# Kernel tuning notes

Hardware: AMD Instinct MI355X
Metric: run time of the kernel (lower is better)

Reference implementation:

```python
import jax, jax.numpy as jnp
import numpy as np

N = 600_000            # active input voxels
CIN, COUT = 64, 128    # IN_CHANNELS, NUM_BEV_FEATURES
B, Z, Y, X = 4, 16, 468, 468  # sparse grid (Waymo-like); conv halves Z
BN_EPS = 1e-5


def setup_inputs() -> dict:
    rng = np.random.default_rng(0)
    # unique active voxel coordinates
    lin = rng.choice(B * Z * Y * X, size=N, replace=False)
    b = lin // (Z * Y * X)
    r = lin % (Z * Y * X)
    z = r // (Y * X)
    r = r % (Y * X)
    y = r // X
    x = r % X
    # spconv rulebook for kernel (2,1,1), stride (2,1,1), pad 0:
    # tap id along z and output segment id from unique (b, z//2, y, x)
    kz = (z % 2).astype(np.int32)
    keys = ((b * (Z // 2) + z // 2) * Y + y) * X + x
    _, inv = np.unique(keys, return_inverse=True)
    out_ids = inv.astype(np.int32)
    n_out = np.int32(out_ids.max() + 1)

    key = jax.random.key(0)
    ks = jax.random.split(key, 6)
    return {
        "features": jax.random.normal(ks[0], (N, CIN), dtype=jnp.float32),
        "W": jax.random.normal(ks[1], (2, CIN, COUT), dtype=jnp.float32) * 0.05,
        "gamma": jax.random.uniform(ks[2], (COUT,), dtype=jnp.float32, minval=0.5, maxval=1.5),
        "beta": jax.random.normal(ks[3], (COUT,), dtype=jnp.float32) * 0.1,
        "running_mean": jax.random.normal(ks[4], (COUT,), dtype=jnp.float32) * 0.1,
        "running_var": jax.random.uniform(ks[5], (COUT,), dtype=jnp.float32, minval=0.5, maxval=1.5),
        "kz": jnp.asarray(kz),
        "out_ids": jnp.asarray(out_ids),
        "n_out": jnp.asarray(n_out),
    }


def reference(features, W, gamma, beta, running_mean, running_var, kz, out_ids, n_out):
    # gather-GEMM: one GEMM per kernel tap, select by tap id
    y0 = features @ W[0]                       # [N, COUT]
    y1 = features @ W[1]
    contrib = jnp.where((kz == 0)[:, None], y0, y1)
    # scatter-add into output voxels (padded to N segments for static shape)
    out = jax.ops.segment_sum(contrib, out_ids, num_segments=N)  # [N, COUT]
    # BatchNorm1d (eval) + ReLU, fused into scatter output pass
    inv_std = gamma * jax.lax.rsqrt(running_var + BN_EPS)
    out = jax.nn.relu((out - running_mean) * inv_std + beta)
    # zero out padding rows beyond the true number of output voxels
    valid = (jnp.arange(N) < n_out)[:, None]
    return jnp.where(valid, out, 0.0)
```

## Files before the change

kernel.cpp:

```cpp
#include <hip/hip_runtime.h>
#include <stdint.h>

#define CIN 64
#define COUT 128
#define TILE_ROWS 64
#define BLOCK 256
#define WT_STRIDE 136
#define A_STRIDE 136

typedef __attribute__((ext_vector_type(8))) __bf16 bf16x8;
typedef __attribute__((ext_vector_type(8))) unsigned short ushort8;
typedef __attribute__((ext_vector_type(4))) float f32x4;

__device__ __forceinline__ unsigned short f2bf(float f) {
    uint32_t u = __float_as_uint(f);
    u = (u + 0x7FFFu + ((u >> 16) & 1u)) >> 16;
    return (unsigned short)u;
}

__global__ void scatter_inv_kernel(const int* __restrict__ kz,
                                   const int* __restrict__ oid,
                                   int* __restrict__ inv0,
                                   int* __restrict__ inv1,
                                   int n) {
    int i = blockIdx.x * blockDim.x + threadIdx.x;
    if (i < n) {
        int o = oid[i];
        if (kz[i] == 0) inv0[o] = i + 1;
        else            inv1[o] = i + 1;
    }
}

__launch_bounds__(BLOCK)
__global__ void spconv_bn_relu_kernel(const float* __restrict__ feat,
                                      const float* __restrict__ W,
                                      const float* __restrict__ gamma,
                                      const float* __restrict__ beta,
                                      const float* __restrict__ rmean,
                                      const float* __restrict__ rvar,
                                      const int* __restrict__ inv0,
                                      const int* __restrict__ inv1,
                                      const int* __restrict__ n_out_p,
                                      float* __restrict__ out,
                                      int N, int num_tiles) {
    __shared__ unsigned short lds_wT[COUT * WT_STRIDE];
    __shared__ unsigned short lds_a[TILE_ROWS * A_STRIDE];
    __shared__ float lds_scale[COUT];
    __shared__ float lds_bias[COUT];

    const int tid = threadIdx.x;
    const int nout = *n_out_p;

    const float4* W4 = (const float4*)W;
    #pragma unroll
    for (int u = 0; u < 16; ++u) {
        int flat4 = u * BLOCK + tid;
        int n4 = flat4 & 31;
        int k  = flat4 >> 5;
        float4 v = W4[flat4];
        int nb = n4 * 4;
        lds_wT[(nb + 0) * WT_STRIDE + k] = f2bf(v.x);
        lds_wT[(nb + 1) * WT_STRIDE + k] = f2bf(v.y);
        lds_wT[(nb + 2) * WT_STRIDE + k] = f2bf(v.z);
        lds_wT[(nb + 3) * WT_STRIDE + k] = f2bf(v.w);
    }
    if (tid < COUT) {
        float s = gamma[tid] * rsqrtf(rvar[tid] + 1e-5f);
        lds_scale[tid] = s;
        lds_bias[tid]  = fmaf(-rmean[tid], s, beta[tid]);
    }
    __syncthreads();

    const float4* feat4 = (const float4*)feat;
    const int wave = tid >> 6;
    const int lane = tid & 63;
    const int lrow = lane & 15;
    const int quad = lane >> 4;

    for (int tile = blockIdx.x; tile < num_tiles; tile += gridDim.x) {
        const int tile_base = tile * TILE_ROWS;

        #pragma unroll
        for (int u = 0; u < 8; ++u) {
            int flat  = u * BLOCK + tid;
            int r     = flat >> 5;
            int rem   = flat & 31;
            int tap   = rem >> 4;
            int chunk = rem & 15;
            int o = tile_base + r;
            int idx = 0;
            if (o < N) idx = tap ? inv1[o] : inv0[o];
            float4 v = make_float4(0.f, 0.f, 0.f, 0.f);
            if (idx > 0) v = feat4[(size_t)(idx - 1) * 16 + chunk];
            uint2 p;
            p.x = (uint32_t)f2bf(v.x) | ((uint32_t)f2bf(v.y) << 16);
            p.y = (uint32_t)f2bf(v.z) | ((uint32_t)f2bf(v.w) << 16);
            *(uint2*)&lds_a[r * A_STRIDE + tap * 64 + chunk * 4] = p;
        }
        __syncthreads();

        const unsigned short* abase = &lds_a[(wave * 16 + lrow) * A_STRIDE + quad * 8];
        bf16x8 afrag[4];
        #pragma unroll
        for (int s = 0; s < 4; ++s)
            afrag[s] = __builtin_bit_cast(bf16x8, *(const ushort8*)(abase + s * 32));

        #pragma unroll
        for (int c = 0; c < 8; ++c) {
            const unsigned short* bbase = &lds_wT[(c * 16 + lrow) * WT_STRIDE + quad * 8];
            f32x4 acc = {0.f, 0.f, 0.f, 0.f};
            #pragma unroll
            for (int s = 0; s < 4; ++s) {
                bf16x8 bfrag = __builtin_bit_cast(bf16x8, *(const ushort8*)(bbase + s * 32));
                acc = __builtin_amdgcn_mfma_f32_16x16x32_bf16(afrag[s], bfrag, acc, 0, 0, 0);
            }
            int col = c * 16 + lrow;
            float sc = lds_scale[col];
            float bi = lds_bias[col];
            int rbase = tile_base + wave * 16 + quad * 4;
            #pragma unroll
            for (int reg = 0; reg < 4; ++reg) {
                int o = rbase + reg;
                if (o < N) {
                    float v = 0.f;
                    if (o < nout) v = fmaxf(fmaf(acc[reg], sc, bi), 0.f);
                    out[(size_t)o * COUT + col] = v;
                }
            }
        }
        __syncthreads();
    }
}

extern "C" void kernel_launch(void* const* d_in, const int* in_sizes, int n_in,
                              void* d_out, int out_size, void* d_ws, size_t ws_size,
                              hipStream_t stream) {
    const float* feat  = (const float*)d_in[0];
    const float* W     = (const float*)d_in[1];
    const float* gamma = (const float*)d_in[2];
    const float* beta  = (const float*)d_in[3];
    const float* rmean = (const float*)d_in[4];
    const float* rvar  = (const float*)d_in[5];
    const int*   kz    = (const int*)d_in[6];
    const int*   oid   = (const int*)d_in[7];
    const int*   noutp = (const int*)d_in[8];
    float* out = (float*)d_out;

    const int N = in_sizes[6];

    int* inv0 = (int*)d_ws;
    int* inv1 = inv0 + N;

    hipMemsetAsync(d_ws, 0, (size_t)2 * N * sizeof(int), stream);

    int sb = (N + 255) / 256;
    scatter_inv_kernel<<<sb, 256, 0, stream>>>(kz, oid, inv0, inv1, N);

    int num_tiles = (N + TILE_ROWS - 1) / TILE_ROWS;
    int grid = num_tiles < 1875 ? num_tiles : 1875;
    spconv_bn_relu_kernel<<<grid, BLOCK, 0, stream>>>(
        feat, W, gamma, beta, rmean, rvar, inv0, inv1, noutp, out, N, num_tiles);
}
```

Before: 558.3 us.

## Gather A fragments directly into registers with software-pipelined per-wave row tiles

The main kernel no longer stages gathered feature rows through LDS with block-wide barriers. Each wave now owns 64 output rows, loads its gather indices up front, and reads feature rows straight into MFMA A-fragment registers. The load of the next 16-row chunk overlaps the MFMAs of the current one. Other changes: the weight tile in LDS uses an XOR swizzle instead of padding, the scatter kernel handles four entries per thread with int4 loads, and the persistent grid becomes one block per 256 rows with launch bounds for occupancy. Costs are higher register pressure and a zero-row pointer taken from workspace for missing taps.

```diff
diff --git a/kernel.cpp b/kernel.cpp
--- a/kernel.cpp
+++ b/kernel.cpp
@@ -3,35 +3,34 @@
 
 #define CIN 64
 #define COUT 128
-#define TILE_ROWS 64
 #define BLOCK 256
-#define WT_STRIDE 136
-#define A_STRIDE 136
+#define ROWS_PER_WAVE 64
 
 typedef __attribute__((ext_vector_type(8))) __bf16 bf16x8;
-typedef __attribute__((ext_vector_type(8))) unsigned short ushort8;
 typedef __attribute__((ext_vector_type(4))) float f32x4;
-
-__device__ __forceinline__ unsigned short f2bf(float f) {
-    uint32_t u = __float_as_uint(f);
-    u = (u + 0x7FFFu + ((u >> 16) & 1u)) >> 16;
-    return (unsigned short)u;
-}
 
 __global__ void scatter_inv_kernel(const int* __restrict__ kz,
                                    const int* __restrict__ oid,
                                    int* __restrict__ inv0,
                                    int* __restrict__ inv1,
                                    int n) {
-    int i = blockIdx.x * blockDim.x + threadIdx.x;
-    if (i < n) {
-        int o = oid[i];
-        if (kz[i] == 0) inv0[o] = i + 1;
-        else            inv1[o] = i + 1;
+    int i = (blockIdx.x * blockDim.x + threadIdx.x) * 4;
+    if (i + 3 < n) {
+        int4 k = *(const int4*)(kz + i);
+        int4 o = *(const int4*)(oid + i);
+        (k.x ? inv1 : inv0)[o.x] = i + 1;
+        (k.y ? inv1 : inv0)[o.y] = i + 2;
+        (k.z ? inv1 : inv0)[o.z] = i + 3;
+        (k.w ? inv1 : inv0)[o.w] = i + 4;
+    } else {
+        for (; i < n; ++i) {
+            if (kz[i]) inv1[oid[i]] = i + 1;
+            else       inv0[oid[i]] = i + 1;
+        }
     }
 }
 
-__launch_bounds__(BLOCK)
+__launch_bounds__(BLOCK, 4)
 __global__ void spconv_bn_relu_kernel(const float* __restrict__ feat,
                                       const float* __restrict__ W,
                                       const float* __restrict__ gamma,
@@ -40,95 +39,109 @@
                                       const float* __restrict__ rvar,
                                       const int* __restrict__ inv0,
                                       const int* __restrict__ inv1,
+                                      const float* __restrict__ zp,
                                       const int* __restrict__ n_out_p,
                                       float* __restrict__ out,
-                                      int N, int num_tiles) {
-    __shared__ unsigned short lds_wT[COUT * WT_STRIDE];
-    __shared__ unsigned short lds_a[TILE_ROWS * A_STRIDE];
-    __shared__ float lds_scale[COUT];
-    __shared__ float lds_bias[COUT];
+                                      int N) {
+    __shared__ unsigned short wT[COUT * 128];
+    __shared__ float s_scale[COUT];
+    __shared__ float s_bias[COUT];
 
     const int tid = threadIdx.x;
-    const int nout = *n_out_p;
 
     const float4* W4 = (const float4*)W;
     #pragma unroll
     for (int u = 0; u < 16; ++u) {
-        int flat4 = u * BLOCK + tid;
-        int n4 = flat4 & 31;
-        int k  = flat4 >> 5;
-        float4 v = W4[flat4];
-        int nb = n4 * 4;
-        lds_wT[(nb + 0) * WT_STRIDE + k] = f2bf(v.x);
-        lds_wT[(nb + 1) * WT_STRIDE + k] = f2bf(v.y);
-        lds_wT[(nb + 2) * WT_STRIDE + k] = f2bf(v.z);
-        lds_wT[(nb + 3) * WT_STRIDE + k] = f2bf(v.w);
+        int f4 = u * BLOCK + tid;
+        int n4 = f4 & 31;
+        int k  = f4 >> 5;
+        float4 v = W4[f4];
+        int kc = k >> 3, jj = k & 7;
+        float vals[4] = {v.x, v.y, v.z, v.w};
+        #pragma unroll
+        for (int e = 0; e < 4; ++e) {
+            int n = n4 * 4 + e;
+            __bf16 h = (__bf16)vals[e];
+            wT[n * 128 + ((kc ^ (n & 7)) << 3) + jj] = __builtin_bit_cast(unsigned short, h);
+        }
     }
     if (tid < COUT) {
         float s = gamma[tid] * rsqrtf(rvar[tid] + 1e-5f);
-        lds_scale[tid] = s;
-        lds_bias[tid]  = fmaf(-rmean[tid], s, beta[tid]);
+        s_scale[tid] = s;
+        s_bias[tid]  = fmaf(-rmean[tid], s, beta[tid]);
     }
     __syncthreads();
 
-    const float4* feat4 = (const float4*)feat;
-    const int wave = tid >> 6;
+    const int nout = *n_out_p;
     const int lane = tid & 63;
-    const int lrow = lane & 15;
-    const int quad = lane >> 4;
+    const int m = lane & 15;
+    const int q = lane >> 4;
+    const int wave_gid = blockIdx.x * 4 + (tid >> 6);
+    const int wbase = wave_gid * ROWS_PER_WAVE;
 
-    for (int tile = blockIdx.x; tile < num_tiles; tile += gridDim.x) {
-        const int tile_base = tile * TILE_ROWS;
+    int idx0[4], idx1[4];
+    #pragma unroll
+    for (int j = 0; j < 4; ++j) {
+        int o = wbase + j * 16 + m;
+        idx0[j] = (o < N) ? inv0[o] : 0;
+        idx1[j] = (o < N) ? inv1[o] : 0;
+    }
 
+    float4 raw[8];
+    bf16x8 af[4];
+
+    auto issue = [&](int j) {
+        const float* p0 = idx0[j] ? feat + (size_t)(idx0[j] - 1) * 64 : zp;
+        const float* p1 = idx1[j] ? feat + (size_t)(idx1[j] - 1) * 64 : zp;
         #pragma unroll
-        for (int u = 0; u < 8; ++u) {
-            int flat  = u * BLOCK + tid;
-            int r     = flat >> 5;
-            int rem   = flat & 31;
-            int tap   = rem >> 4;
-            int chunk = rem & 15;
-            int o = tile_base + r;
-            int idx = 0;
-            if (o < N) idx = tap ? inv1[o] : inv0[o];
-            float4 v = make_float4(0.f, 0.f, 0.f, 0.f);
-            if (idx > 0) v = feat4[(size_t)(idx - 1) * 16 + chunk];
-            uint2 p;
-            p.x = (uint32_t)f2bf(v.x) | ((uint32_t)f2bf(v.y) << 16);
-            p.y = (uint32_t)f2bf(v.z) | ((uint32_t)f2bf(v.w) << 16);
-            *(uint2*)&lds_a[r * A_STRIDE + tap * 64 + chunk * 4] = p;
+        for (int s = 0; s < 4; ++s) {
+            const float* p = (s < 2 ? p0 : p1) + (s & 1) * 32 + q * 8;
+            raw[s * 2 + 0] = *(const float4*)(p);
+            raw[s * 2 + 1] = *(const float4*)(p + 4);
         }
-        __syncthreads();
+    };
 
-        const unsigned short* abase = &lds_a[(wave * 16 + lrow) * A_STRIDE + quad * 8];
-        bf16x8 afrag[4];
+    auto convert = [&]() {
         #pragma unroll
-        for (int s = 0; s < 4; ++s)
-            afrag[s] = __builtin_bit_cast(bf16x8, *(const ushort8*)(abase + s * 32));
+        for (int s = 0; s < 4; ++s) {
+            float4 a = raw[s * 2], b2 = raw[s * 2 + 1];
+            bf16x8 f;
+            f[0] = (__bf16)a.x;  f[1] = (__bf16)a.y;
+            f[2] = (__bf16)a.z;  f[3] = (__bf16)a.w;
+            f[4] = (__bf16)b2.x; f[5] = (__bf16)b2.y;
+            f[6] = (__bf16)b2.z; f[7] = (__bf16)b2.w;
+            af[s] = f;
+        }
+    };
 
+    issue(0);
+    #pragma unroll
+    for (int j = 0; j < 4; ++j) {
+        convert();
+        if (j < 3) issue(j + 1);
+        const int tb = wbase + j * 16;
         #pragma unroll
         for (int c = 0; c < 8; ++c) {
-            const unsigned short* bbase = &lds_wT[(c * 16 + lrow) * WT_STRIDE + quad * 8];
+            const int n = c * 16 + m;
             f32x4 acc = {0.f, 0.f, 0.f, 0.f};
             #pragma unroll
             for (int s = 0; s < 4; ++s) {
-                bf16x8 bfrag = __builtin_bit_cast(bf16x8, *(const ushort8*)(bbase + s * 32));
-                acc = __builtin_amdgcn_mfma_f32_16x16x32_bf16(afrag[s], bfrag, acc, 0, 0, 0);
+                int kc = s * 4 + q;
+                bf16x8 bf = *(const bf16x8*)&wT[n * 128 + ((kc ^ (n & 7)) << 3)];
+                acc = __builtin_amdgcn_mfma_f32_16x16x32_bf16(af[s], bf, acc, 0, 0, 0);
             }
-            int col = c * 16 + lrow;
-            float sc = lds_scale[col];
-            float bi = lds_bias[col];
-            int rbase = tile_base + wave * 16 + quad * 4;
+            const float sc = s_scale[n];
+            const float bi = s_bias[n];
+            const int rb = tb + q * 4;
             #pragma unroll
-            for (int reg = 0; reg < 4; ++reg) {
-                int o = rbase + reg;
+            for (int r = 0; r < 4; ++r) {
+                int o = rb + r;
                 if (o < N) {
-                    float v = 0.f;
-                    if (o < nout) v = fmaxf(fmaf(acc[reg], sc, bi), 0.f);
-                    out[(size_t)o * COUT + col] = v;
+                    float v = (o < nout) ? fmaxf(fmaf(acc[r], sc, bi), 0.f) : 0.f;
+                    out[(size_t)o * COUT + n] = v;
                 }
             }
         }
-        __syncthreads();
     }
 }
 
@@ -150,14 +163,14 @@
 
     int* inv0 = (int*)d_ws;
     int* inv1 = inv0 + N;
+    float* zp = (float*)(inv1 + N);
 
-    hipMemsetAsync(d_ws, 0, (size_t)2 * N * sizeof(int), stream);
+    hipMemsetAsync(d_ws, 0, (size_t)2 * N * sizeof(int) + 64 * sizeof(float), stream);
 
-    int sb = (N + 255) / 256;
+    int sb = (N + 1023) / 1024;
     scatter_inv_kernel<<<sb, 256, 0, stream>>>(kz, oid, inv0, inv1, N);
 
-    int num_tiles = (N + TILE_ROWS - 1) / TILE_ROWS;
-    int grid = num_tiles < 1875 ? num_tiles : 1875;
+    int grid = (N + BLOCK - 1) / BLOCK;
     spconv_bn_relu_kernel<<<grid, BLOCK, 0, stream>>>(
-        feat, W, gamma, beta, rmean, rvar, inv0, inv1, noutp, out, N, num_tiles);
+        feat, W, gamma, beta, rmean, rvar, inv0, inv1, zp, noutp, out, N);
 }
```

New measurement: 608.1 us. 8.9% more time.
